# Kernel tuning notes

Measured on AMD Instinct MI355X. Metric: run time of the kernel, lower is better.

Reference implementation:

```python
import jax, jax.numpy as jnp
import numpy as np

T, H, I, E, Z = 1024, 2048, 1024, 8, 8  # tokens, hidden, moe_intermediate, routed experts, zero experts
TOP_K = 4
ROUTED_SCALING = 1.0


def setup_inputs() -> dict:
    key = jax.random.key(0)
    k0, k1, k2, k3, k4 = jax.random.split(key, 5)
    s = 0.02
    return {
        "hidden_states": jax.random.normal(k0, (T, H), dtype=jnp.float32),
        "router_w": jax.random.normal(k1, (E + Z, H), dtype=jnp.float32) * s,   # classifier weight
        "corr_bias": jnp.zeros((E + Z,), dtype=jnp.float32),                     # e_score_correction_bias
        "w_gate": jax.random.normal(k2, (E, H, I), dtype=jnp.float32) * s,
        "w_up": jax.random.normal(k3, (E, H, I), dtype=jnp.float32) * s,
        "w_down": jax.random.normal(k4, (E, I, H), dtype=jnp.float32) * s,
    }


def reference(hidden_states, router_w, corr_bias, w_gate, w_up, w_down):
    x = hidden_states  # [T, H]
    # ---- router (float32) ----
    logits = x.astype(jnp.float32) @ router_w.T                 # [T, E+Z]
    scores = jax.nn.softmax(logits, axis=-1)
    sel_scores = scores + corr_bias                             # bias used for selection only
    _, topk_idx = jax.lax.top_k(sel_scores, TOP_K)              # [T, K]
    topk_w = jnp.take_along_axis(scores, topk_idx, axis=-1)     # gating weights (renormalize=False)
    topk_w = topk_w * ROUTED_SCALING

    routed = topk_idx < E                                       # [T, K] real-expert mask
    # dense combine weights per routed expert: [T, E]
    onehot = jax.nn.one_hot(jnp.where(routed, topk_idx, 0), E, dtype=x.dtype)
    route_w = jnp.einsum("tke,tk->te", onehot, topk_w * routed.astype(x.dtype))

    # ---- routed experts: silu-gated MLP per expert ----
    gate = jnp.einsum("th,ehi->eti", x, w_gate)                 # [E, T, I]
    up = jnp.einsum("th,ehi->eti", x, w_up)
    mid = jax.nn.silu(gate) * up
    down = jnp.einsum("eti,eih->eth", mid, w_down)              # [E, T, H]
    out = jnp.einsum("te,eth->th", route_w, down)               # combine

    # ---- zero experts (identity type): weight * hidden_states ----
    zero_w = jnp.sum(topk_w * (~routed).astype(x.dtype), axis=-1)  # [T]
    out = out + zero_w[:, None] * x
    return out.astype(hidden_states.dtype)
```

## Files before the change

### kernel.cpp

```cpp
#include <hip/hip_runtime.h>
#include <hip/hip_bf16.h>
#include <math.h>

constexpr int T   = 1024;
constexpr int H   = 2048;
constexpr int I   = 1024;
constexpr int E   = 8;
constexpr int NEZ = 16;
constexpr int TK  = 4;
constexpr int MTG = 24;

typedef short bf16x8 __attribute__((ext_vector_type(8)));
typedef float f32x4  __attribute__((ext_vector_type(4)));
typedef unsigned short u16;
typedef u16 u16x4 __attribute__((ext_vector_type(4)));
typedef u16 u16x8 __attribute__((ext_vector_type(8)));

__device__ __forceinline__ u16 bf16rn(float x) {
  unsigned u = __builtin_bit_cast(unsigned, x);
  u = u + 0x7FFFu + ((u >> 16) & 1u);
  return (u16)(u >> 16);
}
__device__ __forceinline__ float bf16tof(u16 h) {
  return __builtin_bit_cast(float, (unsigned)h << 16);
}

template <int KDIM, int NDIM>
__device__ __forceinline__ void prep_tile(
    const float* __restrict__ src, u16* __restrict__ dh, u16* __restrict__ dl,
    int ei, int kt, int nb)
{
  const int k0 = kt * 32, nn0 = nb * 64;
  __shared__ float Lt[32][65];
  const int tid = threadIdx.x;
#pragma unroll
  for (int r = 0; r < 2; r++) {
    const int f = tid + r * 256;
    const int k = f >> 4, nc = (f & 15) * 4;
    const float4 v = *(const float4*)(src + (size_t)(k0 + k) * NDIM + nn0 + nc);
    Lt[k][nc] = v.x; Lt[k][nc + 1] = v.y; Lt[k][nc + 2] = v.z; Lt[k][nc + 3] = v.w;
  }
  __syncthreads();

  const int w = tid >> 6, lane = tid & 63;
  const int l15 = lane & 15, lg = lane >> 4;
  const int ntg = (nn0 >> 4) + w;
  u16x8 h8, l8;
#pragma unroll
  for (int j = 0; j < 8; j++) {
    const float v = Lt[lg * 8 + j][w * 16 + l15];
    const u16 hh = bf16rn(v);
    h8[j] = hh;
    l8[j] = bf16rn(v - bf16tof(hh));
  }
  const size_t base =
      ((size_t)((size_t)ei * (KDIM >> 5) + kt) * (NDIM >> 4) + ntg) * 512 +
      (size_t)lane * 8;
  *(u16x8*)(dh + base) = h8;
  *(u16x8*)(dl + base) = l8;
}

__global__ __launch_bounds__(256) void prep_gu_kernel(
    const float* __restrict__ wg, const float* __restrict__ wu,
    u16* __restrict__ bgh, u16* __restrict__ bgl,
    u16* __restrict__ buh, u16* __restrict__ bul)
{
  const int z = blockIdx.y;
  const float* src; u16 *dh, *dl;
  if (z < 8) { src = wg + (size_t)z * H * I;       dh = bgh; dl = bgl; }
  else       { src = wu + (size_t)(z - 8) * H * I; dh = buh; dl = bul; }
  prep_tile<H, I>(src, dh, dl, z & 7, blockIdx.x >> 4, blockIdx.x & 15);
}

__global__ __launch_bounds__(256) void prep_d_kernel(
    const float* __restrict__ wd, u16* __restrict__ bdh, u16* __restrict__ bdl)
{
  const int ei = blockIdx.y;
  prep_tile<I, H>(wd + (size_t)ei * I * H, bdh, bdl, ei,
                  blockIdx.x >> 5, blockIdx.x & 31);
}

__global__ __launch_bounds__(256) void prep_a_kernel(
    const float* __restrict__ x, const int* __restrict__ cnt,
    const int* __restrict__ list, u16* __restrict__ Axh, u16* __restrict__ Axl)
{
  const int kt = blockIdx.x;
  const int e  = blockIdx.y;
  int ce = cnt[e]; if (ce > MTG * 16) ce = MTG * 16;
  if (ce == 0) return;
  const int tid = threadIdx.x;
  const int w = tid >> 6, lane = tid & 63;
  const int l15 = lane & 15, lg = lane >> 4;

  for (int mtg = w; mtg < MTG; mtg += 4) {
    int r = mtg * 16 + l15; if (r >= ce) r = ce - 1;
    const int tok = list[e * T + r] >> 2;
    const float* src = x + (size_t)tok * H + kt * 32 + lg * 8;
    const float4 v0 = *(const float4*)(src);
    const float4 v1 = *(const float4*)(src + 4);
    const float vv[8] = {v0.x, v0.y, v0.z, v0.w, v1.x, v1.y, v1.z, v1.w};
    u16x8 h8, l8;
#pragma unroll
    for (int j = 0; j < 8; j++) {
      const u16 hh = bf16rn(vv[j]);
      h8[j] = hh;
      l8[j] = bf16rn(vv[j] - bf16tof(hh));
    }
    const size_t off = (((size_t)e * 64 + kt) * MTG + mtg) * 512 + (size_t)lane * 8;
    *(u16x8*)(Axh + off) = h8;
    *(u16x8*)(Axl + off) = l8;
  }
}

__global__ __launch_bounds__(256) void router_kernel(
    const float* __restrict__ x, const float* __restrict__ rw,
    const float* __restrict__ bias, int* __restrict__ cnt,
    int* __restrict__ list, float* __restrict__ wk4,
    float* __restrict__ zerow)
{
  const int t   = blockIdx.x;
  const int tid = threadIdx.x;
  const float* xt = x + (size_t)t * H;

  float acc[NEZ];
#pragma unroll
  for (int e = 0; e < NEZ; e++) acc[e] = 0.f;

  for (int h = tid; h < H; h += 256) {
    const float xv = xt[h];
#pragma unroll
    for (int e = 0; e < NEZ; e++) acc[e] = fmaf(xv, rw[e * H + h], acc[e]);
  }

#pragma unroll
  for (int e = 0; e < NEZ; e++) {
    float v = acc[e];
#pragma unroll
    for (int off = 32; off >= 1; off >>= 1) v += __shfl_down(v, off, 64);
    acc[e] = v;
  }

  __shared__ float red[4][NEZ];
  const int wv = tid >> 6, ln = tid & 63;
  if (ln == 0) {
#pragma unroll
    for (int e = 0; e < NEZ; e++) red[wv][e] = acc[e];
  }
  __syncthreads();

  if (tid == 0) {
    float l[NEZ];
    float mx = -1e30f;
#pragma unroll
    for (int e = 0; e < NEZ; e++) {
      l[e] = red[0][e] + red[1][e] + red[2][e] + red[3][e];
      mx = fmaxf(mx, l[e]);
    }
    float s = 0.f;
#pragma unroll
    for (int e = 0; e < NEZ; e++) { l[e] = expf(l[e] - mx); s += l[e]; }
    const float inv = 1.f / s;
    float sc[NEZ], sel[NEZ];
#pragma unroll
    for (int e = 0; e < NEZ; e++) {
      sc[e]  = l[e] * inv;
      sel[e] = sc[e] + bias[e];
    }
    float zw = 0.f;
#pragma unroll
    for (int k = 0; k < TK; k++) {
      int best = 0; float bv = sel[0];
#pragma unroll
      for (int e = 1; e < NEZ; e++) {
        if (sel[e] > bv) { bv = sel[e]; best = e; }
      }
      sel[best] = -1e30f;
      const float w = sc[best];
      if (best < E) {
        const int pos = atomicAdd(&cnt[best], 1);
        list[best * T + pos] = (t << 2) | k;
        wk4[t * TK + k] = w;
      } else {
        wk4[t * TK + k] = 0.f;
        zw += w;
      }
    }
    zerow[t] = zw;
  }
}

__global__ __launch_bounds__(256) void gateup_kernel(
    const u16* __restrict__ Axh, const u16* __restrict__ Axl,
    const u16* __restrict__ bgh, const u16* __restrict__ bgl,
    const u16* __restrict__ buh, const u16* __restrict__ bul,
    const int* __restrict__ cnt, const int* __restrict__ list,
    u16* __restrict__ midh, u16* __restrict__ midl)
{
  const int p = blockIdx.x;
  const int L = (p & 7) * 64 + (p >> 3);
  const int e = L >> 6;
  const int rem = L & 63;
  const int n0 = (rem & 31) * 32;
  const int tg = rem >> 5;
  int ce = cnt[e]; if (ce > MTG * 16) ce = MTG * 16;
  if (ce == 0) return;
  const int ntiers = (ce + 63) >> 6;

  const int tid = threadIdx.x;
  const int w = tid >> 6, lane = tid & 63;
  const int l15 = lane & 15, lg = lane >> 4;

  const int tier = tg * 4 + w;
  if (tier >= ntiers) return;

  const size_t bo = ((size_t)e * 64 * 64 + (size_t)(n0 >> 4)) * 1024 + (size_t)lane * 16;
  const char* pBgh = (const char*)bgh + bo;
  const char* pBgl = (const char*)bgl + bo;
  const char* pBuh = (const char*)buh + bo;
  const char* pBul = (const char*)bul + bo;

  const size_t ao = (((size_t)e * 64) * MTG + (size_t)tier * 4) * 1024 + (size_t)lane * 16;
  const char* pAh = (const char*)Axh + ao;
  const char* pAl = (const char*)Axl + ao;

  f32x4 accg[4][2] = {};
  f32x4 accu[4][2] = {};

  bf16x8 A0[8], B0[8], A1[8], B1[8];

#define GU_LOAD(As, Bs, kt_) do {                                         \
    const size_t ka = (size_t)(kt_) * (MTG * 1024);                       \
    const size_t kb = (size_t)(kt_) * 65536;                              \
    _Pragma("unroll") for (int q = 0; q < 4; q++) {                       \
      As[q]     = *(const bf16x8*)(pAh + ka + q * 1024);                  \
      As[4 + q] = *(const bf16x8*)(pAl + ka + q * 1024);                  \
    }                                                                     \
    _Pragma("unroll") for (int j = 0; j < 2; j++) {                       \
      Bs[j * 4 + 0] = *(const bf16x8*)(pBgh + kb + j * 1024);             \
      Bs[j * 4 + 1] = *(const bf16x8*)(pBgl + kb + j * 1024);             \
      Bs[j * 4 + 2] = *(const bf16x8*)(pBuh + kb + j * 1024);             \
      Bs[j * 4 + 3] = *(const bf16x8*)(pBul + kb + j * 1024);             \
    }                                                                     \
  } while (0)

#define GU_STEP(As, Bs) do {                                              \
    _Pragma("unroll") for (int ni = 0; ni < 2; ni++) {                    \
      _Pragma("unroll") for (int mi = 0; mi < 4; mi++) {                  \
        accg[mi][ni] = __builtin_amdgcn_mfma_f32_16x16x32_bf16(As[mi],     Bs[ni*4+0], accg[mi][ni], 0, 0, 0); \
        accg[mi][ni] = __builtin_amdgcn_mfma_f32_16x16x32_bf16(As[mi],     Bs[ni*4+1], accg[mi][ni], 0, 0, 0); \
        accg[mi][ni] = __builtin_amdgcn_mfma_f32_16x16x32_bf16(As[4 + mi], Bs[ni*4+0], accg[mi][ni], 0, 0, 0); \
        accu[mi][ni] = __builtin_amdgcn_mfma_f32_16x16x32_bf16(As[mi],     Bs[ni*4+2], accu[mi][ni], 0, 0, 0); \
        accu[mi][ni] = __builtin_amdgcn_mfma_f32_16x16x32_bf16(As[mi],     Bs[ni*4+3], accu[mi][ni], 0, 0, 0); \
        accu[mi][ni] = __builtin_amdgcn_mfma_f32_16x16x32_bf16(As[4 + mi], Bs[ni*4+2], accu[mi][ni], 0, 0, 0); \
      }                                                                   \
    }                                                                     \
  } while (0)

  GU_LOAD(A0, B0, 0);
  for (int t = 0; t < 64; t += 2) {
    GU_LOAD(A1, B1, t + 1);
    GU_STEP(A0, B0);
    if (t + 2 < 64) GU_LOAD(A0, B0, t + 2);
    GU_STEP(A1, B1);
  }

#pragma unroll
  for (int mi = 0; mi < 4; mi++) {
#pragma unroll
    for (int rr = 0; rr < 4; rr++) {
      const int m = tier * 64 + mi * 16 + lg * 4 + rr;
      if (m >= ce) continue;
#pragma unroll
      for (int ni = 0; ni < 2; ni++) {
        const int n = n0 + ni * 16 + l15;
        const float g = accg[mi][ni][rr];
        const float u = accu[mi][ni][rr];
        const float mv = (g / (1.f + expf(-g))) * u;
        const u16 hh = bf16rn(mv);
        const size_t off =
            (((size_t)e * 32 + (n >> 5)) * MTG + (m >> 4)) * 512 +
            (size_t)((m & 15) + ((n >> 3) & 3) * 16) * 8 + (n & 7);
        midh[off] = hh;
        midl[off] = bf16rn(mv - bf16tof(hh));
      }
    }
  }
#undef GU_LOAD
#undef GU_STEP
}

__global__ __launch_bounds__(256) void down_kernel(
    const u16* __restrict__ midh, const u16* __restrict__ midl,
    const u16* __restrict__ bdh, const u16* __restrict__ bdl,
    const int* __restrict__ cnt, const int* __restrict__ list,
    float* __restrict__ downb)
{
  const int p = blockIdx.x;
  const int L = (p & 7) * 64 + (p >> 3);
  const int e = L >> 6;
  const int rem = L & 63;
  const int n0 = (rem & 31) * 64;
  const int tg = rem >> 5;
  int ce = cnt[e]; if (ce > MTG * 16) ce = MTG * 16;
  if (ce == 0) return;
  const int ntiers = (ce + 63) >> 6;

  const int tid = threadIdx.x;
  const int w = tid >> 6, lane = tid & 63;
  const int l15 = lane & 15, lg = lane >> 4;

  const int tier = tg * 4 + w;
  if (tier >= ntiers) return;

  const size_t bo = ((size_t)e * 32 * 128 + (size_t)(n0 >> 4)) * 1024 + (size_t)lane * 16;
  const char* pBh = (const char*)bdh + bo;
  const char* pBl = (const char*)bdl + bo;

  const size_t ao = (((size_t)e * 32) * MTG + (size_t)tier * 4) * 1024 + (size_t)lane * 16;
  const char* pAh = (const char*)midh + ao;
  const char* pAl = (const char*)midl + ao;

  f32x4 acc[4][4] = {};

  bf16x8 A0[8], B0[8], A1[8], B1[8];

#define DN_LOAD(As, Bs, kt_) do {                                         \
    const size_t ka = (size_t)(kt_) * (MTG * 1024);                       \
    const size_t kb = (size_t)(kt_) * 131072;                             \
    _Pragma("unroll") for (int q = 0; q < 4; q++) {                       \
      As[q]     = *(const bf16x8*)(pAh + ka + q * 1024);                  \
      As[4 + q] = *(const bf16x8*)(pAl + ka + q * 1024);                  \
      Bs[q]     = *(const bf16x8*)(pBh + kb + q * 1024);                  \
      Bs[4 + q] = *(const bf16x8*)(pBl + kb + q * 1024);                  \
    }                                                                     \
  } while (0)

#define DN_STEP(As, Bs) do {                                              \
    _Pragma("unroll") for (int ni = 0; ni < 4; ni++) {                    \
      _Pragma("unroll") for (int mi = 0; mi < 4; mi++) {                  \
        acc[mi][ni] = __builtin_amdgcn_mfma_f32_16x16x32_bf16(As[mi],     Bs[ni],     acc[mi][ni], 0, 0, 0); \
        acc[mi][ni] = __builtin_amdgcn_mfma_f32_16x16x32_bf16(As[mi],     Bs[4 + ni], acc[mi][ni], 0, 0, 0); \
        acc[mi][ni] = __builtin_amdgcn_mfma_f32_16x16x32_bf16(As[4 + mi], Bs[ni],     acc[mi][ni], 0, 0, 0); \
      }                                                                   \
    }                                                                     \
  } while (0)

  DN_LOAD(A0, B0, 0);
  for (int t = 0; t < 32; t += 2) {
    DN_LOAD(A1, B1, t + 1);
    DN_STEP(A0, B0);
    if (t + 2 < 32) DN_LOAD(A0, B0, t + 2);
    DN_STEP(A1, B1);
  }

#pragma unroll
  for (int mi = 0; mi < 4; mi++) {
#pragma unroll
    for (int rr = 0; rr < 4; rr++) {
      const int m = tier * 64 + mi * 16 + lg * 4 + rr;
      if (m >= ce) continue;
      const int ent  = list[e * T + m];
      const int tok  = ent >> 2;
      const int slot = ent & 3;
      float* drow = downb + ((size_t)tok * TK + slot) * H;
#pragma unroll
      for (int ni = 0; ni < 4; ni++) {
        const int n = n0 + ni * 16 + l15;
        drow[n] = acc[mi][ni][rr];
      }
    }
  }
#undef DN_LOAD
#undef DN_STEP
}

__global__ __launch_bounds__(256) void combine_kernel(
    const float* __restrict__ x, const float* __restrict__ downb,
    const float* __restrict__ wk4, const float* __restrict__ zerow,
    float* __restrict__ out)
{
  const int idx = blockIdx.x * 256 + threadIdx.x;
  const int t   = idx >> 9;
  const int h   = (idx & 511) * 4;

  const float w0 = wk4[t * TK + 0];
  const float w1 = wk4[t * TK + 1];
  const float w2 = wk4[t * TK + 2];
  const float w3 = wk4[t * TK + 3];
  const float zw = zerow[t];

  const float4 xv = *(const float4*)(x + (size_t)t * H + h);
  const float4 d0 = *(const float4*)(downb + ((size_t)t * TK + 0) * H + h);
  const float4 d1 = *(const float4*)(downb + ((size_t)t * TK + 1) * H + h);
  const float4 d2 = *(const float4*)(downb + ((size_t)t * TK + 2) * H + h);
  const float4 d3 = *(const float4*)(downb + ((size_t)t * TK + 3) * H + h);

  float4 o;
  o.x = w0 * d0.x + w1 * d1.x + w2 * d2.x + w3 * d3.x + zw * xv.x;
  o.y = w0 * d0.y + w1 * d1.y + w2 * d2.y + w3 * d3.y + zw * xv.y;
  o.z = w0 * d0.z + w1 * d1.z + w2 * d2.z + w3 * d3.z + zw * xv.z;
  o.w = w0 * d0.w + w1 * d1.w + w2 * d2.w + w3 * d3.w + zw * xv.w;
  *(float4*)(out + (size_t)t * H + h) = o;
}

extern "C" void kernel_launch(void* const* d_in, const int* in_sizes, int n_in,
                              void* d_out, int out_size, void* d_ws, size_t ws_size,
                              hipStream_t stream) {
  const float* x    = (const float*)d_in[0];
  const float* rw   = (const float*)d_in[1];
  const float* bias = (const float*)d_in[2];
  const float* wg   = (const float*)d_in[3];
  const float* wu   = (const float*)d_in[4];
  const float* wd   = (const float*)d_in[5];
  float* out = (float*)d_out;

  char* ws = (char*)d_ws;
  size_t off = 0;
  auto alloc = [&](size_t bytes) {
    void* p = ws + off;
    off = (off + bytes + 1023) & ~(size_t)1023;
    return p;
  };
  int*   cnt   = (int*)  alloc(E * sizeof(int));
  int*   list  = (int*)  alloc((size_t)E * T * sizeof(int));
  float* wk4   = (float*)alloc((size_t)T * TK * sizeof(float));
  float* zerow = (float*)alloc((size_t)T * sizeof(float));
  const size_t AXSZ = (size_t)E * 64 * MTG * 512;
  u16*   Axh   = (u16*)  alloc(AXSZ * sizeof(u16));
  u16*   Axl   = (u16*)  alloc(AXSZ * sizeof(u16));
  constexpr size_t PLANE = (size_t)E * H * I * sizeof(u16);
  char*  P     = (char*) alloc(4 * PLANE);
  u16*   bgh   = (u16*)(P);
  u16*   bgl   = (u16*)(P + PLANE);
  u16*   buh   = (u16*)(P + 2 * PLANE);
  u16*   bul   = (u16*)(P + 3 * PLANE);
  u16*   bdh   = bgh;
  u16*   bdl   = bgl;
  float* downb = (float*)(P + 2 * PLANE);
  const size_t MIDSZ = (size_t)E * 32 * MTG * 512;
  u16*   midh  = (u16*)  alloc(MIDSZ * sizeof(u16));
  u16*   midl  = (u16*)  alloc(MIDSZ * sizeof(u16));
  (void)ws_size;

  hipMemsetAsync(cnt, 0, E * sizeof(int), stream);

  router_kernel<<<T, 256, 0, stream>>>(x, rw, bias, cnt, list, wk4, zerow);
  prep_a_kernel<<<dim3(64, 8), 256, 0, stream>>>(x, cnt, list, Axh, Axl);
  prep_gu_kernel<<<dim3(1024, 16), 256, 0, stream>>>(
      wg, wu, bgh, bgl, buh, bul);

  gateup_kernel<<<512, 256, 0, stream>>>(
      Axh, Axl, bgh, bgl, buh, bul, cnt, list, midh, midl);

  prep_d_kernel<<<dim3(1024, 8), 256, 0, stream>>>(wd, bdh, bdl);

  down_kernel<<<512, 256, 0, stream>>>(
      midh, midl, bdh, bdl, cnt, list, downb);
  combine_kernel<<<(T * H / 4) / 256, 256, 0, stream>>>(
      x, downb, wk4, zerow, out);
}
```

Before: 240.5 us.

## Split gate-up K across warp pairs and halve down-proj N tiles

The gate/up kernel now runs 512 threads per block. Two groups of four warps each process half of the K dimension, and the partial accumulators are reduced through shared memory before the SiLU epilogue. The down kernel uses 32-wide N tiles instead of 64 and launches twice as many blocks, with launch bounds hinting at two blocks per CU. Both changes aim to put more waves in flight and hide memory latency, at the cost of an LDS reduction, a block-wide barrier and less reuse of each A tile.

```diff
diff --git a/kernel.cpp b/kernel.cpp
--- a/kernel.cpp
+++ b/kernel.cpp
@@ -189,7 +189,7 @@
   }
 }
 
-__global__ __launch_bounds__(256) void gateup_kernel(
+__global__ __launch_bounds__(512, 2) void gateup_kernel(
     const u16* __restrict__ Axh, const u16* __restrict__ Axl,
     const u16* __restrict__ bgh, const u16* __restrict__ bgl,
     const u16* __restrict__ buh, const u16* __restrict__ bul,
@@ -209,24 +209,29 @@
   const int tid = threadIdx.x;
   const int w = tid >> 6, lane = tid & 63;
   const int l15 = lane & 15, lg = lane >> 4;
-
-  const int tier = tg * 4 + w;
-  if (tier >= ntiers) return;
-
-  const size_t bo = ((size_t)e * 64 * 64 + (size_t)(n0 >> 4)) * 1024 + (size_t)lane * 16;
-  const char* pBgh = (const char*)bgh + bo;
-  const char* pBgl = (const char*)bgl + bo;
-  const char* pBuh = (const char*)buh + bo;
-  const char* pBul = (const char*)bul + bo;
-
-  const size_t ao = (((size_t)e * 64) * MTG + (size_t)tier * 4) * 1024 + (size_t)lane * 16;
-  const char* pAh = (const char*)Axh + ao;
-  const char* pAl = (const char*)Axl + ao;
+  const int tl = w & 3, kh = w >> 2;
+  const int tier = tg * 4 + tl;
+  const bool alive = (tier < ntiers);
+
+  __shared__ float eplds[4][64][68];
 
   f32x4 accg[4][2] = {};
   f32x4 accu[4][2] = {};
 
-  bf16x8 A0[8], B0[8], A1[8], B1[8];
+  if (alive) {
+    const size_t bo = ((size_t)(e * 64 + kh * 32) * 64 + (size_t)(n0 >> 4)) * 1024 +
+                      (size_t)lane * 16;
+    const char* pBgh = (const char*)bgh + bo;
+    const char* pBgl = (const char*)bgl + bo;
+    const char* pBuh = (const char*)buh + bo;
+    const char* pBul = (const char*)bul + bo;
+
+    const size_t ao = (((size_t)(e * 64 + kh * 32)) * MTG + (size_t)tier * 4) * 1024 +
+                      (size_t)lane * 16;
+    const char* pAh = (const char*)Axh + ao;
+    const char* pAl = (const char*)Axl + ao;
+
+    bf16x8 A0[8], B0[8], A1[8], B1[8];
 
 #define GU_LOAD(As, Bs, kt_) do {                                         \
     const size_t ka = (size_t)(kt_) * (MTG * 1024);                       \
@@ -256,51 +261,74 @@
     }                                                                     \
   } while (0)
 
-  GU_LOAD(A0, B0, 0);
-  for (int t = 0; t < 64; t += 2) {
-    GU_LOAD(A1, B1, t + 1);
-    GU_STEP(A0, B0);
-    if (t + 2 < 64) GU_LOAD(A0, B0, t + 2);
-    GU_STEP(A1, B1);
-  }
-
-#pragma unroll
-  for (int mi = 0; mi < 4; mi++) {
-#pragma unroll
-    for (int rr = 0; rr < 4; rr++) {
-      const int m = tier * 64 + mi * 16 + lg * 4 + rr;
-      if (m >= ce) continue;
-#pragma unroll
-      for (int ni = 0; ni < 2; ni++) {
-        const int n = n0 + ni * 16 + l15;
-        const float g = accg[mi][ni][rr];
-        const float u = accu[mi][ni][rr];
-        const float mv = (g / (1.f + expf(-g))) * u;
-        const u16 hh = bf16rn(mv);
-        const size_t off =
-            (((size_t)e * 32 + (n >> 5)) * MTG + (m >> 4)) * 512 +
-            (size_t)((m & 15) + ((n >> 3) & 3) * 16) * 8 + (n & 7);
-        midh[off] = hh;
-        midl[off] = bf16rn(mv - bf16tof(hh));
-      }
-    }
-  }
+    GU_LOAD(A0, B0, 0);
+    for (int t = 0; t < 32; t += 2) {
+      GU_LOAD(A1, B1, t + 1);
+      GU_STEP(A0, B0);
+      if (t + 2 < 32) GU_LOAD(A0, B0, t + 2);
+      GU_STEP(A1, B1);
+    }
 #undef GU_LOAD
 #undef GU_STEP
-}
-
-__global__ __launch_bounds__(256) void down_kernel(
+
+    if (kh == 1) {
+#pragma unroll
+      for (int mi = 0; mi < 4; mi++)
+#pragma unroll
+        for (int ni = 0; ni < 2; ni++) {
+          *(f32x4*)&eplds[tl][lane][(mi * 2 + ni) * 4]      = accg[mi][ni];
+          *(f32x4*)&eplds[tl][lane][32 + (mi * 2 + ni) * 4] = accu[mi][ni];
+        }
+    }
+  }
+
+  __syncthreads();
+
+  if (alive && kh == 0) {
+#pragma unroll
+    for (int mi = 0; mi < 4; mi++)
+#pragma unroll
+      for (int ni = 0; ni < 2; ni++) {
+        accg[mi][ni] += *(const f32x4*)&eplds[tl][lane][(mi * 2 + ni) * 4];
+        accu[mi][ni] += *(const f32x4*)&eplds[tl][lane][32 + (mi * 2 + ni) * 4];
+      }
+
+#pragma unroll
+    for (int mi = 0; mi < 4; mi++) {
+#pragma unroll
+      for (int rr = 0; rr < 4; rr++) {
+        const int m = tier * 64 + mi * 16 + lg * 4 + rr;
+        if (m >= ce) continue;
+#pragma unroll
+        for (int ni = 0; ni < 2; ni++) {
+          const int n = n0 + ni * 16 + l15;
+          const float g = accg[mi][ni][rr];
+          const float u = accu[mi][ni][rr];
+          const float mv = (g / (1.f + expf(-g))) * u;
+          const u16 hh = bf16rn(mv);
+          const size_t off =
+              (((size_t)e * 32 + (n >> 5)) * MTG + (m >> 4)) * 512 +
+              (size_t)((m & 15) + ((n >> 3) & 3) * 16) * 8 + (n & 7);
+          midh[off] = hh;
+          midl[off] = bf16rn(mv - bf16tof(hh));
+        }
+      }
+    }
+  }
+}
+
+__global__ __launch_bounds__(256, 2) void down_kernel(
     const u16* __restrict__ midh, const u16* __restrict__ midl,
     const u16* __restrict__ bdh, const u16* __restrict__ bdl,
     const int* __restrict__ cnt, const int* __restrict__ list,
     float* __restrict__ downb)
 {
   const int p = blockIdx.x;
-  const int L = (p & 7) * 64 + (p >> 3);
-  const int e = L >> 6;
-  const int rem = L & 63;
-  const int n0 = (rem & 31) * 64;
-  const int tg = rem >> 5;
+  const int L = (p & 7) * 128 + (p >> 3);
+  const int e = L >> 7;
+  const int rem = L & 127;
+  const int n0 = (rem & 63) * 32;
+  const int tg = rem >> 6;
   int ce = cnt[e]; if (ce > MTG * 16) ce = MTG * 16;
   if (ce == 0) return;
   const int ntiers = (ce + 63) >> 6;
@@ -320,9 +348,9 @@
   const char* pAh = (const char*)midh + ao;
   const char* pAl = (const char*)midl + ao;
 
-  f32x4 acc[4][4] = {};
-
-  bf16x8 A0[8], B0[8], A1[8], B1[8];
+  f32x4 acc[4][2] = {};
+
+  bf16x8 A0[8], B0[4], A1[8], B1[4];
 
 #define DN_LOAD(As, Bs, kt_) do {                                         \
     const size_t ka = (size_t)(kt_) * (MTG * 1024);                       \
@@ -330,17 +358,19 @@
     _Pragma("unroll") for (int q = 0; q < 4; q++) {                       \
       As[q]     = *(const bf16x8*)(pAh + ka + q * 1024);                  \
       As[4 + q] = *(const bf16x8*)(pAl + ka + q * 1024);                  \
-      Bs[q]     = *(const bf16x8*)(pBh + kb + q * 1024);                  \
-      Bs[4 + q] = *(const bf16x8*)(pBl + kb + q * 1024);                  \
+    }                                                                     \
+    _Pragma("unroll") for (int j = 0; j < 2; j++) {                       \
+      Bs[j * 2 + 0] = *(const bf16x8*)(pBh + kb + j * 1024);              \
+      Bs[j * 2 + 1] = *(const bf16x8*)(pBl + kb + j * 1024);              \
     }                                                                     \
   } while (0)
 
 #define DN_STEP(As, Bs) do {                                              \
-    _Pragma("unroll") for (int ni = 0; ni < 4; ni++) {                    \
+    _Pragma("unroll") for (int ni = 0; ni < 2; ni++) {                    \
       _Pragma("unroll") for (int mi = 0; mi < 4; mi++) {                  \
-        acc[mi][ni] = __builtin_amdgcn_mfma_f32_16x16x32_bf16(As[mi],     Bs[ni],     acc[mi][ni], 0, 0, 0); \
-        acc[mi][ni] = __builtin_amdgcn_mfma_f32_16x16x32_bf16(As[mi],     Bs[4 + ni], acc[mi][ni], 0, 0, 0); \
-        acc[mi][ni] = __builtin_amdgcn_mfma_f32_16x16x32_bf16(As[4 + mi], Bs[ni],     acc[mi][ni], 0, 0, 0); \
+        acc[mi][ni] = __builtin_amdgcn_mfma_f32_16x16x32_bf16(As[mi],     Bs[ni*2+0], acc[mi][ni], 0, 0, 0); \
+        acc[mi][ni] = __builtin_amdgcn_mfma_f32_16x16x32_bf16(As[mi],     Bs[ni*2+1], acc[mi][ni], 0, 0, 0); \
+        acc[mi][ni] = __builtin_amdgcn_mfma_f32_16x16x32_bf16(As[4 + mi], Bs[ni*2+0], acc[mi][ni], 0, 0, 0); \
       }                                                                   \
     }                                                                     \
   } while (0)
@@ -352,6 +382,8 @@
     if (t + 2 < 32) DN_LOAD(A0, B0, t + 2);
     DN_STEP(A1, B1);
   }
+#undef DN_LOAD
+#undef DN_STEP
 
 #pragma unroll
   for (int mi = 0; mi < 4; mi++) {
@@ -364,14 +396,12 @@
       const int slot = ent & 3;
       float* drow = downb + ((size_t)tok * TK + slot) * H;
 #pragma unroll
-      for (int ni = 0; ni < 4; ni++) {
+      for (int ni = 0; ni < 2; ni++) {
         const int n = n0 + ni * 16 + l15;
         drow[n] = acc[mi][ni][rr];
       }
     }
   }
-#undef DN_LOAD
-#undef DN_STEP
 }
 
 __global__ __launch_bounds__(256) void combine_kernel(
@@ -449,12 +479,12 @@
   prep_gu_kernel<<<dim3(1024, 16), 256, 0, stream>>>(
       wg, wu, bgh, bgl, buh, bul);
 
-  gateup_kernel<<<512, 256, 0, stream>>>(
+  gateup_kernel<<<512, 512, 0, stream>>>(
       Axh, Axl, bgh, bgl, buh, bul, cnt, list, midh, midl);
 
   prep_d_kernel<<<dim3(1024, 8), 256, 0, stream>>>(wd, bdh, bdl);
 
-  down_kernel<<<512, 256, 0, stream>>>(
+  down_kernel<<<1024, 256, 0, stream>>>(
       midh, midl, bdh, bdl, cnt, list, downb);
   combine_kernel<<<(T * H / 4) / 256, 256, 0, stream>>>(
       x, downb, wk4, zerow, out);
```

Result: slower. 263.8 us (+9.7%).

## Fuse fp32 weight split-to-bf16 conversion into expert GEMMs via LDS ring

Applied to the files above, without the earlier changes.

Drops the separate prep kernels that converted fp32 expert weights into hi/lo bf16 planes in global memory. Instead each GEMM block loads fp32 weights directly, splits them into hi/lo in registers, and stages them through a triple-buffered LDS ring with barriers. The aim is to avoid writing and then re-reading the full converted weight planes. In exchange, all waves in a block now share one B tile through LDS, which adds barriers and conversion work inside the GEMM loop.

```diff
diff --git a/kernel.cpp b/kernel.cpp
--- a/kernel.cpp
+++ b/kernel.cpp
@@ -13,8 +13,10 @@
 typedef short bf16x8 __attribute__((ext_vector_type(8)));
 typedef float f32x4  __attribute__((ext_vector_type(4)));
 typedef unsigned short u16;
-typedef u16 u16x4 __attribute__((ext_vector_type(4)));
 typedef u16 u16x8 __attribute__((ext_vector_type(8)));
+
+#define SYNC() do { asm volatile("s_waitcnt lgkmcnt(0)" ::: "memory"); \
+                    __builtin_amdgcn_s_barrier(); } while (0)
 
 __device__ __forceinline__ u16 bf16rn(float x) {
   unsigned u = __builtin_bit_cast(unsigned, x);
@@ -23,61 +25,6 @@
 }
 __device__ __forceinline__ float bf16tof(u16 h) {
   return __builtin_bit_cast(float, (unsigned)h << 16);
-}
-
-template <int KDIM, int NDIM>
-__device__ __forceinline__ void prep_tile(
-    const float* __restrict__ src, u16* __restrict__ dh, u16* __restrict__ dl,
-    int ei, int kt, int nb)
-{
-  const int k0 = kt * 32, nn0 = nb * 64;
-  __shared__ float Lt[32][65];
-  const int tid = threadIdx.x;
-#pragma unroll
-  for (int r = 0; r < 2; r++) {
-    const int f = tid + r * 256;
-    const int k = f >> 4, nc = (f & 15) * 4;
-    const float4 v = *(const float4*)(src + (size_t)(k0 + k) * NDIM + nn0 + nc);
-    Lt[k][nc] = v.x; Lt[k][nc + 1] = v.y; Lt[k][nc + 2] = v.z; Lt[k][nc + 3] = v.w;
-  }
-  __syncthreads();
-
-  const int w = tid >> 6, lane = tid & 63;
-  const int l15 = lane & 15, lg = lane >> 4;
-  const int ntg = (nn0 >> 4) + w;
-  u16x8 h8, l8;
-#pragma unroll
-  for (int j = 0; j < 8; j++) {
-    const float v = Lt[lg * 8 + j][w * 16 + l15];
-    const u16 hh = bf16rn(v);
-    h8[j] = hh;
-    l8[j] = bf16rn(v - bf16tof(hh));
-  }
-  const size_t base =
-      ((size_t)((size_t)ei * (KDIM >> 5) + kt) * (NDIM >> 4) + ntg) * 512 +
-      (size_t)lane * 8;
-  *(u16x8*)(dh + base) = h8;
-  *(u16x8*)(dl + base) = l8;
-}
-
-__global__ __launch_bounds__(256) void prep_gu_kernel(
-    const float* __restrict__ wg, const float* __restrict__ wu,
-    u16* __restrict__ bgh, u16* __restrict__ bgl,
-    u16* __restrict__ buh, u16* __restrict__ bul)
-{
-  const int z = blockIdx.y;
-  const float* src; u16 *dh, *dl;
-  if (z < 8) { src = wg + (size_t)z * H * I;       dh = bgh; dl = bgl; }
-  else       { src = wu + (size_t)(z - 8) * H * I; dh = buh; dl = bul; }
-  prep_tile<H, I>(src, dh, dl, z & 7, blockIdx.x >> 4, blockIdx.x & 15);
-}
-
-__global__ __launch_bounds__(256) void prep_d_kernel(
-    const float* __restrict__ wd, u16* __restrict__ bdh, u16* __restrict__ bdl)
-{
-  const int ei = blockIdx.y;
-  prep_tile<I, H>(wd + (size_t)ei * I * H, bdh, bdl, ei,
-                  blockIdx.x >> 5, blockIdx.x & 31);
 }
 
 __global__ __launch_bounds__(256) void prep_a_kernel(
@@ -191,8 +138,7 @@
 
 __global__ __launch_bounds__(256) void gateup_kernel(
     const u16* __restrict__ Axh, const u16* __restrict__ Axl,
-    const u16* __restrict__ bgh, const u16* __restrict__ bgl,
-    const u16* __restrict__ buh, const u16* __restrict__ bul,
+    const float* __restrict__ wg, const float* __restrict__ wu,
     const int* __restrict__ cnt, const int* __restrict__ list,
     u16* __restrict__ midh, u16* __restrict__ midl)
 {
@@ -200,69 +146,102 @@
   const int L = (p & 7) * 64 + (p >> 3);
   const int e = L >> 6;
   const int rem = L & 63;
-  const int n0 = (rem & 31) * 32;
+  const int nu = rem & 31;
   const int tg = rem >> 5;
+  const int n0 = nu * 32;
   int ce = cnt[e]; if (ce > MTG * 16) ce = MTG * 16;
   if (ce == 0) return;
   const int ntiers = (ce + 63) >> 6;
+  if (tg == 1 && ntiers <= 4) return;
+
+  __shared__ __align__(16) char ldsB[3][8192];
 
   const int tid = threadIdx.x;
   const int w = tid >> 6, lane = tid & 63;
   const int l15 = lane & 15, lg = lane >> 4;
-
   const int tier = tg * 4 + w;
-  if (tier >= ntiers) return;
-
-  const size_t bo = ((size_t)e * 64 * 64 + (size_t)(n0 >> 4)) * 1024 + (size_t)lane * 16;
-  const char* pBgh = (const char*)bgh + bo;
-  const char* pBgl = (const char*)bgl + bo;
-  const char* pBuh = (const char*)buh + bo;
-  const char* pBul = (const char*)bul + bo;
-
-  const size_t ao = (((size_t)e * 64) * MTG + (size_t)tier * 4) * 1024 + (size_t)lane * 16;
-  const char* pAh = (const char*)Axh + ao;
-  const char* pAl = (const char*)Axl + ao;
+  const bool alive = (tier < ntiers);
+
+  const int mat = tid >> 7;
+  const int oct = (tid >> 5) & 3;
+  const int nl  = tid & 31;
+  const int ntgw = nl >> 4;
+  const int Lw   = (nl & 15) | (oct << 4);
+  const int foh  = ((mat << 2) | ntgw) * 1024 + Lw * 16;
+  const float* wsrc = (mat ? wu : wg) + (size_t)e * H * I +
+                      (size_t)(oct * 8) * I + (size_t)(n0 + nl);
+
+  const int mt0 = (tier <= 5) ? tier * 4 : MTG - 4;
+  const char* pAh = (const char*)Axh + (((size_t)e * 64) * MTG + mt0) * 1024 + (size_t)lane * 16;
+  const char* pAl = (const char*)Axl + (((size_t)e * 64) * MTG + mt0) * 1024 + (size_t)lane * 16;
 
   f32x4 accg[4][2] = {};
   f32x4 accu[4][2] = {};
-
-  bf16x8 A0[8], B0[8], A1[8], B1[8];
-
-#define GU_LOAD(As, Bs, kt_) do {                                         \
-    const size_t ka = (size_t)(kt_) * (MTG * 1024);                       \
-    const size_t kb = (size_t)(kt_) * 65536;                              \
+  bf16x8 a0[8], a1[8], a2[8];
+  float s0[8], s1[8], s2[8];
+
+#define GU_ISSUE(S, KT) do {                                              \
+    const float* ps_ = wsrc + (size_t)(KT) * (32 * (size_t)I);            \
+    _Pragma("unroll") for (int j = 0; j < 8; j++) S[j] = ps_[(size_t)j * I]; \
+  } while (0)
+
+#define GU_ALOAD(A, KT) do {                                              \
+    const size_t ka_ = (size_t)(KT) * (MTG * 1024);                       \
     _Pragma("unroll") for (int q = 0; q < 4; q++) {                       \
-      As[q]     = *(const bf16x8*)(pAh + ka + q * 1024);                  \
-      As[4 + q] = *(const bf16x8*)(pAl + ka + q * 1024);                  \
-    }                                                                     \
-    _Pragma("unroll") for (int j = 0; j < 2; j++) {                       \
-      Bs[j * 4 + 0] = *(const bf16x8*)(pBgh + kb + j * 1024);             \
-      Bs[j * 4 + 1] = *(const bf16x8*)(pBgl + kb + j * 1024);             \
-      Bs[j * 4 + 2] = *(const bf16x8*)(pBuh + kb + j * 1024);             \
-      Bs[j * 4 + 3] = *(const bf16x8*)(pBul + kb + j * 1024);             \
-    }                                                                     \
-  } while (0)
-
-#define GU_STEP(As, Bs) do {                                              \
-    _Pragma("unroll") for (int ni = 0; ni < 2; ni++) {                    \
+      A[q]     = *(const bf16x8*)(pAh + ka_ + q * 1024);                  \
+      A[4 + q] = *(const bf16x8*)(pAl + ka_ + q * 1024);                  \
+    } } while (0)
+
+#define GU_CONVW(S, WB) do {                                              \
+    u16x8 h8_, l8_;                                                       \
+    _Pragma("unroll") for (int j = 0; j < 8; j++) {                       \
+      const u16 hh_ = bf16rn(S[j]);                                       \
+      h8_[j] = hh_; l8_[j] = bf16rn(S[j] - bf16tof(hh_)); }               \
+    *(u16x8*)(&ldsB[WB][0] + foh) = h8_;                                  \
+    *(u16x8*)(&ldsB[WB][0] + foh + 2048) = l8_;                           \
+  } while (0)
+
+#define GU_COMP(RB, A) do {                                               \
+    const char* bp_ = &ldsB[RB][0];                                       \
+    _Pragma("unroll") for (int ntg = 0; ntg < 2; ntg++) {                 \
+      const bf16x8 ggh = *(const bf16x8*)(bp_ + ntg * 1024        + lane * 16); \
+      const bf16x8 ggl = *(const bf16x8*)(bp_ + ntg * 1024 + 2048 + lane * 16); \
+      const bf16x8 guh = *(const bf16x8*)(bp_ + ntg * 1024 + 4096 + lane * 16); \
+      const bf16x8 gul = *(const bf16x8*)(bp_ + ntg * 1024 + 6144 + lane * 16); \
       _Pragma("unroll") for (int mi = 0; mi < 4; mi++) {                  \
-        accg[mi][ni] = __builtin_amdgcn_mfma_f32_16x16x32_bf16(As[mi],     Bs[ni*4+0], accg[mi][ni], 0, 0, 0); \
-        accg[mi][ni] = __builtin_amdgcn_mfma_f32_16x16x32_bf16(As[mi],     Bs[ni*4+1], accg[mi][ni], 0, 0, 0); \
-        accg[mi][ni] = __builtin_amdgcn_mfma_f32_16x16x32_bf16(As[4 + mi], Bs[ni*4+0], accg[mi][ni], 0, 0, 0); \
-        accu[mi][ni] = __builtin_amdgcn_mfma_f32_16x16x32_bf16(As[mi],     Bs[ni*4+2], accu[mi][ni], 0, 0, 0); \
-        accu[mi][ni] = __builtin_amdgcn_mfma_f32_16x16x32_bf16(As[mi],     Bs[ni*4+3], accu[mi][ni], 0, 0, 0); \
-        accu[mi][ni] = __builtin_amdgcn_mfma_f32_16x16x32_bf16(As[4 + mi], Bs[ni*4+2], accu[mi][ni], 0, 0, 0); \
-      }                                                                   \
-    }                                                                     \
-  } while (0)
-
-  GU_LOAD(A0, B0, 0);
-  for (int t = 0; t < 64; t += 2) {
-    GU_LOAD(A1, B1, t + 1);
-    GU_STEP(A0, B0);
-    if (t + 2 < 64) GU_LOAD(A0, B0, t + 2);
-    GU_STEP(A1, B1);
-  }
+        accg[mi][ntg] = __builtin_amdgcn_mfma_f32_16x16x32_bf16(A[mi],     ggh, accg[mi][ntg], 0, 0, 0); \
+        accg[mi][ntg] = __builtin_amdgcn_mfma_f32_16x16x32_bf16(A[mi],     ggl, accg[mi][ntg], 0, 0, 0); \
+        accg[mi][ntg] = __builtin_amdgcn_mfma_f32_16x16x32_bf16(A[4 + mi], ggh, accg[mi][ntg], 0, 0, 0); \
+        accu[mi][ntg] = __builtin_amdgcn_mfma_f32_16x16x32_bf16(A[mi],     guh, accu[mi][ntg], 0, 0, 0); \
+        accu[mi][ntg] = __builtin_amdgcn_mfma_f32_16x16x32_bf16(A[mi],     gul, accu[mi][ntg], 0, 0, 0); \
+        accu[mi][ntg] = __builtin_amdgcn_mfma_f32_16x16x32_bf16(A[4 + mi], guh, accu[mi][ntg], 0, 0, 0); \
+      } } } while (0)
+
+#define GU_BODY(K, SI, AU, AN, SC, RB, WB) do {                           \
+    const int k_ = (K);                                                   \
+    SYNC();                                                               \
+    if (k_ + 3 < 64) GU_ISSUE(SI, k_ + 3);                                \
+    if (k_ + 1 < 64) GU_ALOAD(AN, k_ + 1);                                \
+    if (alive) GU_COMP(RB, AU);                                           \
+    if (k_ + 1 < 64) GU_CONVW(SC, WB);                                    \
+  } while (0)
+
+  GU_ISSUE(s0, 0); GU_ISSUE(s1, 1); GU_ISSUE(s2, 2);
+  GU_ALOAD(a0, 0);
+  GU_CONVW(s0, 0);
+
+  for (int kb = 0; kb < 63; kb += 3) {
+    GU_BODY(kb,     s0, a0, a1, s1, 0, 1);
+    GU_BODY(kb + 1, s1, a1, a2, s2, 1, 2);
+    GU_BODY(kb + 2, s2, a2, a0, s0, 2, 0);
+  }
+  GU_BODY(63, s0, a0, a1, s1, 0, 1);
+
+#undef GU_ISSUE
+#undef GU_ALOAD
+#undef GU_CONVW
+#undef GU_COMP
+#undef GU_BODY
 
 #pragma unroll
   for (int mi = 0; mi < 4; mi++) {
@@ -271,10 +250,10 @@
       const int m = tier * 64 + mi * 16 + lg * 4 + rr;
       if (m >= ce) continue;
 #pragma unroll
-      for (int ni = 0; ni < 2; ni++) {
-        const int n = n0 + ni * 16 + l15;
-        const float g = accg[mi][ni][rr];
-        const float u = accu[mi][ni][rr];
+      for (int ntg = 0; ntg < 2; ntg++) {
+        const int n = n0 + ntg * 16 + l15;
+        const float g = accg[mi][ntg][rr];
+        const float u = accu[mi][ntg][rr];
         const float mv = (g / (1.f + expf(-g))) * u;
         const u16 hh = bf16rn(mv);
         const size_t off =
@@ -285,13 +264,11 @@
       }
     }
   }
-#undef GU_LOAD
-#undef GU_STEP
 }
 
 __global__ __launch_bounds__(256) void down_kernel(
     const u16* __restrict__ midh, const u16* __restrict__ midl,
-    const u16* __restrict__ bdh, const u16* __restrict__ bdl,
+    const float* __restrict__ wd,
     const int* __restrict__ cnt, const int* __restrict__ list,
     float* __restrict__ downb)
 {
@@ -299,59 +276,96 @@
   const int L = (p & 7) * 64 + (p >> 3);
   const int e = L >> 6;
   const int rem = L & 63;
-  const int n0 = (rem & 31) * 64;
+  const int nu = rem & 31;
   const int tg = rem >> 5;
+  const int n0 = nu * 64;
   int ce = cnt[e]; if (ce > MTG * 16) ce = MTG * 16;
   if (ce == 0) return;
   const int ntiers = (ce + 63) >> 6;
+  if (tg == 1 && ntiers <= 4) return;
+
+  __shared__ __align__(16) char ldsB[3][8192];
 
   const int tid = threadIdx.x;
   const int w = tid >> 6, lane = tid & 63;
   const int l15 = lane & 15, lg = lane >> 4;
-
   const int tier = tg * 4 + w;
-  if (tier >= ntiers) return;
-
-  const size_t bo = ((size_t)e * 32 * 128 + (size_t)(n0 >> 4)) * 1024 + (size_t)lane * 16;
-  const char* pBh = (const char*)bdh + bo;
-  const char* pBl = (const char*)bdl + bo;
-
-  const size_t ao = (((size_t)e * 32) * MTG + (size_t)tier * 4) * 1024 + (size_t)lane * 16;
-  const char* pAh = (const char*)midh + ao;
-  const char* pAl = (const char*)midl + ao;
+  const bool alive = (tier < ntiers);
+
+  const int oct = tid >> 6;
+  const int nl  = tid & 63;
+  const int ntgw = nl >> 4;
+  const int Lw   = (nl & 15) | (oct << 4);
+  const int foh  = ntgw * 1024 + Lw * 16;
+  const float* wsrc = wd + (size_t)e * I * H +
+                      (size_t)(oct * 8) * H + (size_t)(n0 + nl);
+
+  const int mt0 = (tier <= 5) ? tier * 4 : MTG - 4;
+  const char* pAh = (const char*)midh + (((size_t)e * 32) * MTG + mt0) * 1024 + (size_t)lane * 16;
+  const char* pAl = (const char*)midl + (((size_t)e * 32) * MTG + mt0) * 1024 + (size_t)lane * 16;
 
   f32x4 acc[4][4] = {};
-
-  bf16x8 A0[8], B0[8], A1[8], B1[8];
-
-#define DN_LOAD(As, Bs, kt_) do {                                         \
-    const size_t ka = (size_t)(kt_) * (MTG * 1024);                       \
-    const size_t kb = (size_t)(kt_) * 131072;                             \
+  bf16x8 a0[8], a1[8], a2[8];
+  float s0[8], s1[8], s2[8];
+
+#define DN_ISSUE(S, KT) do {                                              \
+    const float* ps_ = wsrc + (size_t)(KT) * (32 * (size_t)H);            \
+    _Pragma("unroll") for (int j = 0; j < 8; j++) S[j] = ps_[(size_t)j * H]; \
+  } while (0)
+
+#define DN_ALOAD(A, KT) do {                                              \
+    const size_t ka_ = (size_t)(KT) * (MTG * 1024);                       \
     _Pragma("unroll") for (int q = 0; q < 4; q++) {                       \
-      As[q]     = *(const bf16x8*)(pAh + ka + q * 1024);                  \
-      As[4 + q] = *(const bf16x8*)(pAl + ka + q * 1024);                  \
-      Bs[q]     = *(const bf16x8*)(pBh + kb + q * 1024);                  \
-      Bs[4 + q] = *(const bf16x8*)(pBl + kb + q * 1024);                  \
-    }                                                                     \
-  } while (0)
-
-#define DN_STEP(As, Bs) do {                                              \
-    _Pragma("unroll") for (int ni = 0; ni < 4; ni++) {                    \
+      A[q]     = *(const bf16x8*)(pAh + ka_ + q * 1024);                  \
+      A[4 + q] = *(const bf16x8*)(pAl + ka_ + q * 1024);                  \
+    } } while (0)
+
+#define DN_CONVW(S, WB) do {                                              \
+    u16x8 h8_, l8_;                                                       \
+    _Pragma("unroll") for (int j = 0; j < 8; j++) {                       \
+      const u16 hh_ = bf16rn(S[j]);                                       \
+      h8_[j] = hh_; l8_[j] = bf16rn(S[j] - bf16tof(hh_)); }               \
+    *(u16x8*)(&ldsB[WB][0] + foh) = h8_;                                  \
+    *(u16x8*)(&ldsB[WB][0] + foh + 4096) = l8_;                           \
+  } while (0)
+
+#define DN_COMP(RB, A) do {                                               \
+    const char* bp_ = &ldsB[RB][0];                                       \
+    _Pragma("unroll") for (int ntg = 0; ntg < 4; ntg++) {                 \
+      const bf16x8 bh = *(const bf16x8*)(bp_ + ntg * 1024        + lane * 16); \
+      const bf16x8 bl = *(const bf16x8*)(bp_ + ntg * 1024 + 4096 + lane * 16); \
       _Pragma("unroll") for (int mi = 0; mi < 4; mi++) {                  \
-        acc[mi][ni] = __builtin_amdgcn_mfma_f32_16x16x32_bf16(As[mi],     Bs[ni],     acc[mi][ni], 0, 0, 0); \
-        acc[mi][ni] = __builtin_amdgcn_mfma_f32_16x16x32_bf16(As[mi],     Bs[4 + ni], acc[mi][ni], 0, 0, 0); \
-        acc[mi][ni] = __builtin_amdgcn_mfma_f32_16x16x32_bf16(As[4 + mi], Bs[ni],     acc[mi][ni], 0, 0, 0); \
-      }                                                                   \
-    }                                                                     \
-  } while (0)
-
-  DN_LOAD(A0, B0, 0);
-  for (int t = 0; t < 32; t += 2) {
-    DN_LOAD(A1, B1, t + 1);
-    DN_STEP(A0, B0);
-    if (t + 2 < 32) DN_LOAD(A0, B0, t + 2);
-    DN_STEP(A1, B1);
-  }
+        acc[mi][ntg] = __builtin_amdgcn_mfma_f32_16x16x32_bf16(A[mi],     bh, acc[mi][ntg], 0, 0, 0); \
+        acc[mi][ntg] = __builtin_amdgcn_mfma_f32_16x16x32_bf16(A[mi],     bl, acc[mi][ntg], 0, 0, 0); \
+        acc[mi][ntg] = __builtin_amdgcn_mfma_f32_16x16x32_bf16(A[4 + mi], bh, acc[mi][ntg], 0, 0, 0); \
+      } } } while (0)
+
+#define DN_BODY(K, SI, AU, AN, SC, RB, WB) do {                           \
+    const int k_ = (K);                                                   \
+    SYNC();                                                               \
+    if (k_ + 3 < 32) DN_ISSUE(SI, k_ + 3);                                \
+    if (k_ + 1 < 32) DN_ALOAD(AN, k_ + 1);                                \
+    if (alive) DN_COMP(RB, AU);                                           \
+    if (k_ + 1 < 32) DN_CONVW(SC, WB);                                    \
+  } while (0)
+
+  DN_ISSUE(s0, 0); DN_ISSUE(s1, 1); DN_ISSUE(s2, 2);
+  DN_ALOAD(a0, 0);
+  DN_CONVW(s0, 0);
+
+  for (int kb = 0; kb < 30; kb += 3) {
+    DN_BODY(kb,     s0, a0, a1, s1, 0, 1);
+    DN_BODY(kb + 1, s1, a1, a2, s2, 1, 2);
+    DN_BODY(kb + 2, s2, a2, a0, s0, 2, 0);
+  }
+  DN_BODY(30, s0, a0, a1, s1, 0, 1);
+  DN_BODY(31, s1, a1, a2, s2, 1, 2);
+
+#undef DN_ISSUE
+#undef DN_ALOAD
+#undef DN_CONVW
+#undef DN_COMP
+#undef DN_BODY
 
 #pragma unroll
   for (int mi = 0; mi < 4; mi++) {
@@ -364,14 +378,12 @@
       const int slot = ent & 3;
       float* drow = downb + ((size_t)tok * TK + slot) * H;
 #pragma unroll
-      for (int ni = 0; ni < 4; ni++) {
-        const int n = n0 + ni * 16 + l15;
-        drow[n] = acc[mi][ni][rr];
+      for (int ntg = 0; ntg < 4; ntg++) {
+        const int n = n0 + ntg * 16 + l15;
+        drow[n] = acc[mi][ntg][rr];
       }
     }
   }
-#undef DN_LOAD
-#undef DN_STEP
 }
 
 __global__ __launch_bounds__(256) void combine_kernel(
@@ -428,34 +440,23 @@
   const size_t AXSZ = (size_t)E * 64 * MTG * 512;
   u16*   Axh   = (u16*)  alloc(AXSZ * sizeof(u16));
   u16*   Axl   = (u16*)  alloc(AXSZ * sizeof(u16));
-  constexpr size_t PLANE = (size_t)E * H * I * sizeof(u16);
-  char*  P     = (char*) alloc(4 * PLANE);
-  u16*   bgh   = (u16*)(P);
-  u16*   bgl   = (u16*)(P + PLANE);
-  u16*   buh   = (u16*)(P + 2 * PLANE);
-  u16*   bul   = (u16*)(P + 3 * PLANE);
-  u16*   bdh   = bgh;
-  u16*   bdl   = bgl;
-  float* downb = (float*)(P + 2 * PLANE);
   const size_t MIDSZ = (size_t)E * 32 * MTG * 512;
   u16*   midh  = (u16*)  alloc(MIDSZ * sizeof(u16));
   u16*   midl  = (u16*)  alloc(MIDSZ * sizeof(u16));
+  float* downb = (float*)alloc((size_t)T * TK * H * sizeof(float));
   (void)ws_size;
 
   hipMemsetAsync(cnt, 0, E * sizeof(int), stream);
 
   router_kernel<<<T, 256, 0, stream>>>(x, rw, bias, cnt, list, wk4, zerow);
   prep_a_kernel<<<dim3(64, 8), 256, 0, stream>>>(x, cnt, list, Axh, Axl);
-  prep_gu_kernel<<<dim3(1024, 16), 256, 0, stream>>>(
-      wg, wu, bgh, bgl, buh, bul);
 
   gateup_kernel<<<512, 256, 0, stream>>>(
-      Axh, Axl, bgh, bgl, buh, bul, cnt, list, midh, midl);
-
-  prep_d_kernel<<<dim3(1024, 8), 256, 0, stream>>>(wd, bdh, bdl);
+      Axh, Axl, wg, wu, cnt, list, midh, midl);
 
   down_kernel<<<512, 256, 0, stream>>>(
-      midh, midl, bdh, bdl, cnt, list, downb);
+      midh, midl, wd, cnt, list, downb);
+
   combine_kernel<<<(T * H / 4) / 256, 256, 0, stream>>>(
       x, downb, wk4, zerow, out);
 }
```

After: 199.0 us (median of 3 runs). 1.21x faster.
